# Performance work log

Measured on AMD Instinct MI355X. Metric: run time of the kernel, lower is better.

## Reference

```python
import jax, jax.numpy as jnp
import numpy as np

N_NODES = 50000
N_EDGES = 800000
N_GRAPHS = 512
IN_DIM = 128
HID = 256
K = 4
D4 = HID // K  # 64
OUT_DIM = 2
LN_EPS = 1e-5
BN_EPS = 1e-5


def elu(x):
    return jnp.where(x > 0, x, jnp.expm1(x))


def gin_conv(x, src, dst, n, W1, b1, W2, b2):
    # PyG GINConv, eps=0: mlp(x + sum_{j->i} x_j); mlp = Linear->ReLU->Linear
    agg = x + jax.ops.segment_sum(x[src], dst, num_segments=n)
    h = jnp.maximum(agg @ W1 + b1, 0.0)
    return h @ W2 + b2


def full_layernorm(x):
    # LayerNorm(normalized_shape=x.size(), elementwise_affine=False):
    # normalizes over the ENTIRE tensor (all nodes+features jointly)
    m = x.mean()
    v = x.var()  # biased, matches torch LayerNorm
    return (x - m) * jax.lax.rsqrt(v + LN_EPS)


def bn_eval(h):
    # BatchNorm1d in eval mode with fresh running stats (mean=0, var=1, affine=1/0)
    return h * jax.lax.rsqrt(jnp.float32(1.0) + BN_EPS)


def setup_inputs():
    key = jax.random.key(0)
    ks = jax.random.split(key, 24)
    rn = lambda k, shape, s=0.05: jax.random.normal(k, shape, dtype=jnp.float32) * s
    return {
        "x": jax.random.normal(ks[0], (N_NODES, IN_DIM), dtype=jnp.float32),
        "edge_index": jax.random.randint(ks[1], (2, N_EDGES), 0, N_NODES, dtype=jnp.int32),
        "batch": jnp.sort(jax.random.randint(ks[2], (N_NODES,), 0, N_GRAPHS, dtype=jnp.int32)),
        "lin1_W": rn(ks[3], (IN_DIM, HID)),
        "lin1_b": rn(ks[4], (HID,)),
        "gin0_W1": rn(ks[5], (HID, HID)),
        "gin0_b1": rn(ks[6], (HID,)),
        "gin0_W2": rn(ks[7], (HID, HID)),
        "gin0_b2": rn(ks[8], (HID,)),
        "gin1_W1": rn(ks[9], (K, D4, D4)),
        "gin1_b1": rn(ks[10], (K, D4)),
        "gin1_W2": rn(ks[11], (K, D4, D4)),
        "gin1_b2": rn(ks[12], (K, D4)),
        "vn_emb": jnp.zeros((HID,), dtype=jnp.float32),  # init constant 0
        "vn_W1": rn(ks[13], (HID, 2 * HID)),
        "vn_b1": rn(ks[14], (2 * HID,)),
        "vn_W2": rn(ks[15], (2 * HID, HID)),
        "vn_b2": rn(ks[16], (HID,)),
        "lin_out_W": rn(ks[17], (HID * 2 * 3, HID)),
        "lin_out_b": rn(ks[18], (HID,)),
        "cls_W": rn(ks[19], (HID, OUT_DIM)),
        "cls_b": rn(ks[20], (OUT_DIM,)),
        "dh_W": rn(ks[21], (3, D4)),
        "dh_b": rn(ks[22], (3,)),
    }


def reference(x, edge_index, batch, lin1_W, lin1_b,
              gin0_W1, gin0_b1, gin0_W2, gin0_b2,
              gin1_W1, gin1_b1, gin1_W2, gin1_b2,
              vn_emb, vn_W1, vn_b1, vn_W2, vn_b2,
              lin_out_W, lin_out_b, cls_W, cls_b, dh_W, dh_b):
    n = x.shape[0]
    # edge_attr is None -> add self loops
    src = jnp.concatenate([edge_index[0], jnp.arange(n, dtype=edge_index.dtype)])
    dst = jnp.concatenate([edge_index[1], jnp.arange(n, dtype=edge_index.dtype)])

    h = elu(x @ lin1_W + lin1_b)                       # [N, HID]
    vn = jnp.broadcast_to(vn_emb, (N_GRAPHS, HID))     # virtualnode embedding per graph

    gr = [h]
    # ---- layer 0: NaSingleOp (full-width GIN) ----
    orix = h
    h = h + vn[batch]
    h = gin_conv(h, src, dst, n, gin0_W1, gin0_b1, gin0_W2, gin0_b2)
    h = full_layernorm(elu(h))
    gr.append(h)
    # virtual node update (i < num_layers - 1)
    vt = jax.ops.segment_sum(orix, batch, num_segments=N_GRAPHS) + vn
    vn = jnp.maximum(bn_eval(vt @ vn_W1 + vn_b1), 0.0)
    vn = jnp.maximum(bn_eval(vn @ vn_W2 + vn_b2), 0.0)

    # ---- layer 1: NaDisenOp (4 quarter-width GINs on hsplit chunks) ----
    h = h + vn[batch]
    hk = h.reshape(n, K, D4)                           # hsplit(4)
    zk = jax.vmap(
        lambda xi, W1, b1, W2, b2: gin_conv(xi, src, dst, n, W1, b1, W2, b2),
        in_axes=(1, 0, 0, 0, 0), out_axes=1,
    )(hk, gin1_W1, gin1_b1, gin1_W2, gin1_b2)          # [N, K, D4]
    h = zk.reshape(n, HID)                             # hstack
    h = full_layernorm(elu(h))
    gr.append(h)

    gr = jnp.concatenate(gr, axis=1)                   # [N, 3*HID]

    # Pooling_trivial: passthrough. Readout_trivial: cat(max_pool, mean_pool)
    mx = jax.ops.segment_max(gr, batch, num_segments=N_GRAPHS)
    counts = jax.ops.segment_sum(jnp.ones((n,), dtype=gr.dtype), batch, num_segments=N_GRAPHS)
    mean = jax.ops.segment_sum(gr, batch, num_segments=N_GRAPHS) / jnp.maximum(counts, 1.0)[:, None]
    read = jnp.concatenate([mx, mean], axis=1)         # [G, 6*HID]

    x5 = elu(read @ lin_out_W + lin_out_b)             # [G, HID]

    # Disen3Head: first 3 of 4 hsplit chunks -> Linear(D4,1) -> 0.05+0.35*sigmoid
    xs = x5.reshape(N_GRAPHS, K, D4)
    z = jnp.einsum('gkd,kd->gk', xs[:, :3, :], dh_W) + dh_b
    ssl = 0.05 + 0.35 * jax.nn.sigmoid(z)              # [G, 3]

    logits = jax.nn.log_softmax(x5 @ cls_W + cls_b, axis=-1)  # mol=False
    return (logits, x5, ssl)
```

## Files before the change

### kernel.cpp

```cpp
#include <hip/hip_runtime.h>

static constexpr int NG = 512;
static constexpr float LN_EPS = 1e-5f;
static constexpr float BNS = 0.9999950000374997f;

__device__ __forceinline__ float eluf(float v) { return v > 0.f ? v : expm1f(v); }

typedef __attribute__((ext_vector_type(8))) short bf16x8;
typedef __attribute__((ext_vector_type(4))) float f32x4;

__device__ __forceinline__ ushort f2b(float f) {
    union { float f; unsigned u; } v; v.f = f;
    const unsigned u = v.u;
    return (ushort)((u + 0x7FFFu + ((u >> 16) & 1u)) >> 16);
}
__device__ __forceinline__ float b2f(ushort b) {
    union { unsigned u; float f; } v; v.u = ((unsigned)b) << 16;
    return v.f;
}

__device__ __forceinline__ void gl16(const ushort* g, ushort* l) {
    __builtin_amdgcn_global_load_lds(
        (const __attribute__((address_space(1))) void*)g,
        (__attribute__((address_space(3))) void*)l, 16, 0, 0);
}

template<int KSTEPS>
__global__ __launch_bounds__(512)
void tgemm_kernel(const ushort* __restrict__ Ab, int ldab,
                  const ushort* __restrict__ Wt,
                  const float* __restrict__ bias,
                  ushort* __restrict__ Cb,
                  int n)
{
    __shared__ __align__(16) ushort sbuf[32768];
    ushort* As = sbuf;
    ushort* Bs = sbuf + 8192;

    const int tid = threadIdx.x;
    const int lane = tid & 63;
    const int wv = tid >> 6;
    const int wr = wv >> 1, wc = wv & 1;
    const int r0 = blockIdx.x * 128;
    const int colL = lane & 15;
    const int lr = lane >> 4;

    f32x4 acc[2][8];
#pragma unroll
    for (int rt = 0; rt < 2; ++rt)
#pragma unroll
        for (int ct = 0; ct < 8; ++ct) acc[rt][ct] = (f32x4){0.f, 0.f, 0.f, 0.f};

    for (int ks = 0; ks < KSTEPS; ++ks) {
#pragma unroll
        for (int it = 0; it < 2; ++it) {
            const int i = it * 512 + tid;
            const int row = i >> 3, cb = i & 7;
            const int rg = min(r0 + row, n - 1);
            gl16(Ab + (size_t)rg * ldab + ks * 64 + ((cb ^ (row & 7)) * 8), As + i * 8);
        }
#pragma unroll
        for (int it = 0; it < 4; ++it) {
            const int i = it * 512 + tid;
            const int col = i >> 3, cb = i & 7;
            gl16(Wt + (size_t)col * (KSTEPS * 64) + ks * 64 + ((cb ^ (col & 7)) * 8), Bs + i * 8);
        }
        __syncthreads();

        bf16x8 af[2][2];
#pragma unroll
        for (int rt = 0; rt < 2; ++rt)
#pragma unroll
            for (int kk = 0; kk < 2; ++kk) {
                const int row = wr * 32 + rt * 16 + colL;
                const int blk = kk * 4 + lr;
                af[rt][kk] = *reinterpret_cast<const bf16x8*>(As + row * 64 + ((blk ^ (row & 7)) * 8));
            }
#pragma unroll
        for (int ct = 0; ct < 8; ++ct)
#pragma unroll
            for (int kk = 0; kk < 2; ++kk) {
                const int col = wc * 128 + ct * 16 + colL;
                const int blk = kk * 4 + lr;
                const bf16x8 bf = *reinterpret_cast<const bf16x8*>(Bs + col * 64 + ((blk ^ (col & 7)) * 8));
                acc[0][ct] = __builtin_amdgcn_mfma_f32_16x16x32_bf16(af[0][kk], bf, acc[0][ct], 0, 0, 0);
                acc[1][ct] = __builtin_amdgcn_mfma_f32_16x16x32_bf16(af[1][kk], bf, acc[1][ct], 0, 0, 0);
            }
        __syncthreads();
    }

    float bv[8];
#pragma unroll
    for (int ct = 0; ct < 8; ++ct) bv[ct] = bias[wc * 128 + ct * 16 + colL];

    ushort* eb = sbuf + wv * 4096;
#pragma unroll
    for (int rt = 0; rt < 2; ++rt)
#pragma unroll
        for (int ct = 0; ct < 8; ++ct)
#pragma unroll
            for (int r = 0; r < 4; ++r) {
                const float v = eluf(acc[rt][ct][r] + bv[ct]);
                eb[(rt * 16 + lr * 4 + r) * 128 + ct * 16 + colL] = f2b(v);
            }
#pragma unroll
    for (int j = 0; j < 8; ++j) {
        const int idx = j * 64 + lane;
        const int lrow = idx >> 4, c8 = idx & 15;
        const int grow = r0 + wr * 32 + lrow;
        if (grow < n)
            *reinterpret_cast<bf16x8*>(Cb + (size_t)grow * 256 + wc * 128 + c8 * 8) =
                *reinterpret_cast<const bf16x8*>(eb + lrow * 128 + c8 * 8);
    }
}

__global__ __launch_bounds__(512)
void mlp0_kernel(const ushort* __restrict__ Ab,
                 const ushort* __restrict__ W1t,
                 const ushort* __restrict__ W2t,
                 const float* __restrict__ b1, const float* __restrict__ b2,
                 ushort* __restrict__ Cb,
                 int n, double* __restrict__ stats)
{
    __shared__ __align__(16) ushort As[8192];
    __shared__ __align__(16) ushort Bs[16384];
    __shared__ __align__(16) ushort Z[32768];

    const int tid = threadIdx.x;
    const int lane = tid & 63;
    const int wv = tid >> 6;
    const int wr = wv >> 1, wc = wv & 1;
    const int r0 = blockIdx.x * 128;
    const int colL = lane & 15;
    const int lr = lane >> 4;

    f32x4 acc[2][8];
#pragma unroll
    for (int rt = 0; rt < 2; ++rt)
#pragma unroll
        for (int ct = 0; ct < 8; ++ct) acc[rt][ct] = (f32x4){0.f, 0.f, 0.f, 0.f};

    for (int ks = 0; ks < 4; ++ks) {
#pragma unroll
        for (int it = 0; it < 2; ++it) {
            const int i = it * 512 + tid;
            const int row = i >> 3, cb = i & 7;
            const int rg = min(r0 + row, n - 1);
            gl16(Ab + (size_t)rg * 256 + ks * 64 + ((cb ^ (row & 7)) * 8), As + i * 8);
        }
#pragma unroll
        for (int it = 0; it < 4; ++it) {
            const int i = it * 512 + tid;
            const int col = i >> 3, cb = i & 7;
            gl16(W1t + (size_t)col * 256 + ks * 64 + ((cb ^ (col & 7)) * 8), Bs + i * 8);
        }
        __syncthreads();
        bf16x8 af[2][2];
#pragma unroll
        for (int rt = 0; rt < 2; ++rt)
#pragma unroll
            for (int kk = 0; kk < 2; ++kk) {
                const int row = wr * 32 + rt * 16 + colL;
                const int blk = kk * 4 + lr;
                af[rt][kk] = *reinterpret_cast<const bf16x8*>(As + row * 64 + ((blk ^ (row & 7)) * 8));
            }
#pragma unroll
        for (int ct = 0; ct < 8; ++ct)
#pragma unroll
            for (int kk = 0; kk < 2; ++kk) {
                const int col = wc * 128 + ct * 16 + colL;
                const int blk = kk * 4 + lr;
                const bf16x8 bf = *reinterpret_cast<const bf16x8*>(Bs + col * 64 + ((blk ^ (col & 7)) * 8));
                acc[0][ct] = __builtin_amdgcn_mfma_f32_16x16x32_bf16(af[0][kk], bf, acc[0][ct], 0, 0, 0);
                acc[1][ct] = __builtin_amdgcn_mfma_f32_16x16x32_bf16(af[1][kk], bf, acc[1][ct], 0, 0, 0);
            }
        __syncthreads();
    }
#pragma unroll
    for (int ct = 0; ct < 8; ++ct) {
        const float bvv = b1[wc * 128 + ct * 16 + colL];
#pragma unroll
        for (int rt = 0; rt < 2; ++rt)
#pragma unroll
            for (int r = 0; r < 4; ++r) {
                const float v = fmaxf(acc[rt][ct][r] + bvv, 0.f);
                const int zrow = wr * 32 + rt * 16 + lr * 4 + r;
                const int zcol = wc * 128 + ct * 16 + colL;
                const int chunk = zcol >> 3;
                const int sw = (chunk & 24) | ((chunk & 7) ^ (zrow & 7));
                Z[zrow * 256 + sw * 8 + (zcol & 7)] = f2b(v);
            }
    }
    __syncthreads();

#pragma unroll
    for (int rt = 0; rt < 2; ++rt)
#pragma unroll
        for (int ct = 0; ct < 8; ++ct) acc[rt][ct] = (f32x4){0.f, 0.f, 0.f, 0.f};

    for (int ks = 0; ks < 4; ++ks) {
#pragma unroll
        for (int it = 0; it < 4; ++it) {
            const int i = it * 512 + tid;
            const int col = i >> 3, cb = i & 7;
            gl16(W2t + (size_t)col * 256 + ks * 64 + ((cb ^ (col & 7)) * 8), Bs + i * 8);
        }
        __syncthreads();
        bf16x8 zf[2][2];
#pragma unroll
        for (int rt = 0; rt < 2; ++rt)
#pragma unroll
            for (int kk = 0; kk < 2; ++kk) {
                const int zrow = wr * 32 + rt * 16 + colL;
                const int chunk = ks * 8 + kk * 4 + lr;
                const int sw = (chunk & 24) | ((chunk & 7) ^ (zrow & 7));
                zf[rt][kk] = *reinterpret_cast<const bf16x8*>(Z + zrow * 256 + sw * 8);
            }
#pragma unroll
        for (int ct = 0; ct < 8; ++ct)
#pragma unroll
            for (int kk = 0; kk < 2; ++kk) {
                const int col = wc * 128 + ct * 16 + colL;
                const int blk = kk * 4 + lr;
                const bf16x8 bf = *reinterpret_cast<const bf16x8*>(Bs + col * 64 + ((blk ^ (col & 7)) * 8));
                acc[0][ct] = __builtin_amdgcn_mfma_f32_16x16x32_bf16(zf[0][kk], bf, acc[0][ct], 0, 0, 0);
                acc[1][ct] = __builtin_amdgcn_mfma_f32_16x16x32_bf16(zf[1][kk], bf, acc[1][ct], 0, 0, 0);
            }
        __syncthreads();
    }

    float bv[8];
#pragma unroll
    for (int ct = 0; ct < 8; ++ct) bv[ct] = b2[wc * 128 + ct * 16 + colL];
    ushort* eb = Z + wv * 4096;
    float s = 0.f, ss = 0.f;
#pragma unroll
    for (int rt = 0; rt < 2; ++rt)
#pragma unroll
        for (int ct = 0; ct < 8; ++ct)
#pragma unroll
            for (int r = 0; r < 4; ++r) {
                const float v = eluf(acc[rt][ct][r] + bv[ct]);
                eb[(rt * 16 + lr * 4 + r) * 128 + ct * 16 + colL] = f2b(v);
                const int row = r0 + wr * 32 + rt * 16 + lr * 4 + r;
                if (row < n) { s += v; ss += v * v; }
            }
#pragma unroll
    for (int j = 0; j < 8; ++j) {
        const int idx = j * 64 + lane;
        const int lrow = idx >> 4, c8 = idx & 15;
        const int grow = r0 + wr * 32 + lrow;
        if (grow < n)
            *reinterpret_cast<bf16x8*>(Cb + (size_t)grow * 256 + wc * 128 + c8 * 8) =
                *reinterpret_cast<const bf16x8*>(eb + lrow * 128 + c8 * 8);
    }
    double ds = (double)s, dss = (double)ss;
    for (int o = 32; o; o >>= 1) { ds += __shfl_down(ds, o, 64); dss += __shfl_down(dss, o, 64); }
    if (lane == 0) {
        const int bkt = (blockIdx.x & 63) * 2;
        unsafeAtomicAdd(&stats[bkt], ds); unsafeAtomicAdd(&stats[bkt + 1], dss);
    }
}

__global__ __launch_bounds__(256)
void bd2_kernel(const ushort* __restrict__ Ab,
                const ushort* __restrict__ W1t,
                const ushort* __restrict__ W2t,
                const float* __restrict__ b1, const float* __restrict__ b2,
                ushort* __restrict__ Cb,
                int n, double* __restrict__ stats)
{
    __shared__ __align__(16) ushort As[8192];
    __shared__ __align__(16) ushort B1s[4096];
    __shared__ __align__(16) ushort B2s[4096];

    const int tid = threadIdx.x;
    const int lane = tid & 63;
    const int wv = tid >> 6;
    const int ch = blockIdx.y;
    const int r0 = blockIdx.x * 128;
    const int colL = lane & 15;
    const int lr = lane >> 4;

#pragma unroll
    for (int it = 0; it < 4; ++it) {
        const int i = it * 256 + tid;
        const int row = i >> 3, cb = i & 7;
        const int rg = min(r0 + row, n - 1);
        gl16(Ab + (size_t)rg * 256 + ch * 64 + ((cb ^ (row & 7)) * 8), As + i * 8);
    }
#pragma unroll
    for (int it = 0; it < 2; ++it) {
        const int i = it * 256 + tid;
        const int col = i >> 3, cb = i & 7;
        gl16(W1t + ch * 4096 + col * 64 + ((cb ^ (col & 7)) * 8), B1s + i * 8);
    }
#pragma unroll
    for (int it = 0; it < 2; ++it) {
        const int i = it * 256 + tid;
        const int col = i >> 3, cb = i & 7;
        gl16(W2t + ch * 4096 + col * 64 + ((cb ^ (col & 7)) * 8), B2s + i * 8);
    }
    __syncthreads();

    bf16x8 af[2][2];
#pragma unroll
    for (int rt = 0; rt < 2; ++rt)
#pragma unroll
        for (int kk = 0; kk < 2; ++kk) {
            const int row = wv * 32 + rt * 16 + colL;
            const int blk = kk * 4 + lr;
            af[rt][kk] = *reinterpret_cast<const bf16x8*>(As + row * 64 + ((blk ^ (row & 7)) * 8));
        }
    f32x4 acc[2][4];
#pragma unroll
    for (int rt = 0; rt < 2; ++rt)
#pragma unroll
        for (int ct = 0; ct < 4; ++ct) acc[rt][ct] = (f32x4){0.f, 0.f, 0.f, 0.f};
#pragma unroll
    for (int ct = 0; ct < 4; ++ct)
#pragma unroll
        for (int kk = 0; kk < 2; ++kk) {
            const int col = ct * 16 + colL;
            const int blk = kk * 4 + lr;
            const bf16x8 bf = *reinterpret_cast<const bf16x8*>(B1s + col * 64 + ((blk ^ (col & 7)) * 8));
            acc[0][ct] = __builtin_amdgcn_mfma_f32_16x16x32_bf16(af[0][kk], bf, acc[0][ct], 0, 0, 0);
            acc[1][ct] = __builtin_amdgcn_mfma_f32_16x16x32_bf16(af[1][kk], bf, acc[1][ct], 0, 0, 0);
        }

    ushort* Zw = As + wv * 2048;
#pragma unroll
    for (int rt = 0; rt < 2; ++rt)
#pragma unroll
        for (int ct = 0; ct < 4; ++ct) {
            const float bvv = b1[ch * 64 + ct * 16 + colL];
#pragma unroll
            for (int r = 0; r < 4; ++r) {
                const float v = fmaxf(acc[rt][ct][r] + bvv, 0.f);
                const int zrow = rt * 16 + lr * 4 + r;
                const int zcol = ct * 16 + colL;
                Zw[zrow * 64 + (((zcol >> 3) ^ (zrow & 7)) * 8) + (zcol & 7)] = f2b(v);
            }
        }

    bf16x8 zf[2][2];
#pragma unroll
    for (int rt = 0; rt < 2; ++rt)
#pragma unroll
        for (int kk = 0; kk < 2; ++kk) {
            const int zrow = rt * 16 + colL;
            const int blk = kk * 4 + lr;
            zf[rt][kk] = *reinterpret_cast<const bf16x8*>(Zw + zrow * 64 + ((blk ^ (zrow & 7)) * 8));
        }
#pragma unroll
    for (int rt = 0; rt < 2; ++rt)
#pragma unroll
        for (int ct = 0; ct < 4; ++ct) acc[rt][ct] = (f32x4){0.f, 0.f, 0.f, 0.f};
#pragma unroll
    for (int ct = 0; ct < 4; ++ct)
#pragma unroll
        for (int kk = 0; kk < 2; ++kk) {
            const int col = ct * 16 + colL;
            const int blk = kk * 4 + lr;
            const bf16x8 bf = *reinterpret_cast<const bf16x8*>(B2s + col * 64 + ((blk ^ (col & 7)) * 8));
            acc[0][ct] = __builtin_amdgcn_mfma_f32_16x16x32_bf16(zf[0][kk], bf, acc[0][ct], 0, 0, 0);
            acc[1][ct] = __builtin_amdgcn_mfma_f32_16x16x32_bf16(zf[1][kk], bf, acc[1][ct], 0, 0, 0);
        }

    float s = 0.f, ss = 0.f;
#pragma unroll
    for (int rt = 0; rt < 2; ++rt)
#pragma unroll
        for (int ct = 0; ct < 4; ++ct) {
            const float bvv = b2[ch * 64 + ct * 16 + colL];
#pragma unroll
            for (int r = 0; r < 4; ++r) {
                const float v = eluf(acc[rt][ct][r] + bvv);
                Zw[(rt * 16 + lr * 4 + r) * 64 + ct * 16 + colL] = f2b(v);
                const int row = r0 + wv * 32 + rt * 16 + lr * 4 + r;
                if (row < n) { s += v; ss += v * v; }
            }
        }
#pragma unroll
    for (int j = 0; j < 4; ++j) {
        const int idx = j * 64 + lane;
        const int lrow = idx >> 3, c8 = idx & 7;
        const int grow = r0 + wv * 32 + lrow;
        if (grow < n)
            *reinterpret_cast<bf16x8*>(Cb + (size_t)grow * 256 + ch * 64 + c8 * 8) =
                *reinterpret_cast<const bf16x8*>(Zw + lrow * 64 + c8 * 8);
    }

    double ds = (double)s, dss = (double)ss;
    for (int o = 32; o; o >>= 1) { ds += __shfl_down(ds, o, 64); dss += __shfl_down(dss, o, 64); }
    if (lane == 0) {
        const int bkt = ((blockIdx.x + blockIdx.y * 16) & 63) * 2;
        unsafeAtomicAdd(&stats[bkt], ds); unsafeAtomicAdd(&stats[bkt + 1], dss);
    }
}

__global__ __launch_bounds__(64)
void finalize_kernel(const double* __restrict__ sacc, float* __restrict__ sfin, double M)
{
    const int t = threadIdx.x;
    double s = sacc[t * 2], ss = sacc[t * 2 + 1];
    for (int o = 32; o; o >>= 1) { s += __shfl_down(s, o, 64); ss += __shfl_down(ss, o, 64); }
    if (t == 0) {
        const double mean = s / M;
        double var = ss / M - mean * mean;
        if (var < 0.0) var = 0.0;
        sfin[0] = (float)mean;
        sfin[1] = (float)(1.0 / sqrt(var + (double)LN_EPS));
    }
}

__global__ void prep_kernel(const float* __restrict__ x,
                            const float* __restrict__ lin1W,
                            const float* __restrict__ g0W1, const float* __restrict__ g0W2,
                            const float* __restrict__ g1W1, const float* __restrict__ g1W2,
                            ushort* __restrict__ xb,
                            ushort* __restrict__ Wt1,
                            ushort* __restrict__ Wt0a, ushort* __restrict__ Wt0b,
                            ushort* __restrict__ Wtbd1, ushort* __restrict__ Wtbd2,
                            int n32)
{
    const int i = blockIdx.x * 256 + threadIdx.x;
    if (i < n32) {
        const float4 v = reinterpret_cast<const float4*>(x)[i];
        reinterpret_cast<ushort4*>(xb)[i] = make_ushort4(f2b(v.x), f2b(v.y), f2b(v.z), f2b(v.w));
        return;
    }
    int j = i - n32;
    if (j < 32768) {
        const int c = j >> 7, k = j & 127;
        Wt1[j] = f2b(lin1W[(size_t)k * 256 + c]);
    } else if (j < 98304) {
        j -= 32768;
        const int c = j >> 8, k = j & 255;
        Wt0a[j] = f2b(g0W1[(size_t)k * 256 + c]);
    } else if (j < 163840) {
        j -= 98304;
        const int c = j >> 8, k = j & 255;
        Wt0b[j] = f2b(g0W2[(size_t)k * 256 + c]);
    } else if (j < 180224) {
        j -= 163840;
        const int ch = j >> 12, r = j & 4095, cw = r >> 6, k = r & 63;
        Wtbd1[j] = f2b(g1W1[ch * 4096 + k * 64 + cw]);
    } else if (j < 196608) {
        j -= 180224;
        const int ch = j >> 12, r = j & 4095, cw = r >> 6, k = r & 63;
        Wtbd2[j] = f2b(g1W2[ch * 4096 + k * 64 + cw]);
    }
}

__global__ void count_kernel(const int* __restrict__ dst, int* __restrict__ cnt, int nE)
{
    const int e = blockIdx.x * 256 + threadIdx.x;
    if (e < nE) atomicAdd(&cnt[dst[e]], 1);
}

__global__ __launch_bounds__(256)
void scan1_kernel(const int* __restrict__ cnt, int* __restrict__ bsum, int n)
{
    __shared__ int ws[4];
    const int i = blockIdx.x * 256 + threadIdx.x;
    int v = (i < n) ? cnt[i] : 0;
    for (int o = 32; o; o >>= 1) v += __shfl_down(v, o, 64);
    if ((threadIdx.x & 63) == 0) ws[threadIdx.x >> 6] = v;
    __syncthreads();
    if (threadIdx.x == 0) bsum[blockIdx.x] = ws[0] + ws[1] + ws[2] + ws[3];
}

__global__ __launch_bounds__(256)
void scan2_kernel(int* __restrict__ bsum, int* __restrict__ rowptr, int nb, int n)
{
    __shared__ int sh[256];
    const int t = threadIdx.x;
    const int v = (t < nb) ? bsum[t] : 0;
    sh[t] = v;
    __syncthreads();
    for (int o = 1; o < 256; o <<= 1) {
        const int u = (t >= o) ? sh[t - o] : 0;
        __syncthreads();
        sh[t] += u;
        __syncthreads();
    }
    if (t < nb) bsum[t] = sh[t] - v;
    if (t == 255) rowptr[n] = sh[255];
}

__global__ __launch_bounds__(256)
void scan3_kernel(const int* __restrict__ cnt, const int* __restrict__ bsum,
                  int* __restrict__ rowptr, int* __restrict__ cursor, int n)
{
    __shared__ int sh[256];
    const int t = threadIdx.x;
    const int i = blockIdx.x * 256 + t;
    const int v = (i < n) ? cnt[i] : 0;
    sh[t] = v;
    __syncthreads();
    for (int o = 1; o < 256; o <<= 1) {
        const int u = (t >= o) ? sh[t - o] : 0;
        __syncthreads();
        sh[t] += u;
        __syncthreads();
    }
    if (i < n) {
        const int ex = bsum[blockIdx.x] + sh[t] - v;
        rowptr[i] = ex;
        cursor[i] = ex;
    }
}

__global__ void fill_kernel(const int* __restrict__ src, const int* __restrict__ dst,
                            int* __restrict__ cursor, int* __restrict__ es, int nE)
{
    const int e = blockIdx.x * 256 + threadIdx.x;
    if (e >= nE) return;
    const int p = atomicAdd(&cursor[dst[e]], 1);
    es[p] = src[e];
}

__global__ __launch_bounds__(256)
void gather0b_kernel(const ushort* __restrict__ hb, const int* __restrict__ rowptr,
                     const int* __restrict__ es, const float* __restrict__ vn_emb,
                     ushort* __restrict__ ob, int n)
{
    const int node = blockIdx.x * 4 + (threadIdx.x >> 6);
    if (node >= n) return;
    const int lane = threadIdx.x & 63;
    const ushort4* H4 = reinterpret_cast<const ushort4*>(hb);
    const ushort4 o = H4[(size_t)node * 64 + lane];
    const int b = rowptr[node], e = rowptr[node + 1];
    const float4 vn = reinterpret_cast<const float4*>(vn_emb)[lane];
    const float cv = (float)(2 + (e - b));
    float a0 = fmaf(cv, vn.x, 2.f * b2f(o.x));
    float a1 = fmaf(cv, vn.y, 2.f * b2f(o.y));
    float a2 = fmaf(cv, vn.z, 2.f * b2f(o.z));
    float a3 = fmaf(cv, vn.w, 2.f * b2f(o.w));
    int i = b;
    for (; i + 2 <= e; i += 2) {
        const ushort4 v0 = H4[(size_t)es[i] * 64 + lane];
        const ushort4 v1 = H4[(size_t)es[i + 1] * 64 + lane];
        a0 += b2f(v0.x) + b2f(v1.x);
        a1 += b2f(v0.y) + b2f(v1.y);
        a2 += b2f(v0.z) + b2f(v1.z);
        a3 += b2f(v0.w) + b2f(v1.w);
    }
    for (; i < e; ++i) {
        const ushort4 v = H4[(size_t)es[i] * 64 + lane];
        a0 += b2f(v.x); a1 += b2f(v.y); a2 += b2f(v.z); a3 += b2f(v.w);
    }
    reinterpret_cast<ushort4*>(ob)[(size_t)node * 64 + lane] =
        make_ushort4(f2b(a0), f2b(a1), f2b(a2), f2b(a3));
}

__global__ __launch_bounds__(256)
void gatherb_kernel(const ushort* __restrict__ tb, const int* __restrict__ rowptr,
                    const int* __restrict__ es, ushort* __restrict__ ob, int n)
{
    const int node = blockIdx.x * 4 + (threadIdx.x >> 6);
    if (node >= n) return;
    const int lane = threadIdx.x & 63;
    const ushort4* H4 = reinterpret_cast<const ushort4*>(tb);
    const ushort4 o = H4[(size_t)node * 64 + lane];
    float a0 = 2.f * b2f(o.x), a1 = 2.f * b2f(o.y), a2 = 2.f * b2f(o.z), a3 = 2.f * b2f(o.w);
    const int b = rowptr[node], e = rowptr[node + 1];
    int i = b;
    for (; i + 2 <= e; i += 2) {
        const ushort4 v0 = H4[(size_t)es[i] * 64 + lane];
        const ushort4 v1 = H4[(size_t)es[i + 1] * 64 + lane];
        a0 += b2f(v0.x) + b2f(v1.x);
        a1 += b2f(v0.y) + b2f(v1.y);
        a2 += b2f(v0.z) + b2f(v1.z);
        a3 += b2f(v0.w) + b2f(v1.w);
    }
    for (; i < e; ++i) {
        const ushort4 v = H4[(size_t)es[i] * 64 + lane];
        a0 += b2f(v.x); a1 += b2f(v.y); a2 += b2f(v.z); a3 += b2f(v.w);
    }
    reinterpret_cast<ushort4*>(ob)[(size_t)node * 64 + lane] =
        make_ushort4(f2b(a0), f2b(a1), f2b(a2), f2b(a3));
}

__global__ void offsets_kernel(const int* __restrict__ batch, int n, int* __restrict__ off)
{
    const int g = blockIdx.x * blockDim.x + threadIdx.x;
    if (g > NG) return;
    int lo = 0, hi = n;
    while (lo < hi) { const int mid = (lo + hi) >> 1; if (batch[mid] < g) lo = mid + 1; else hi = mid; }
    off[g] = lo;
}

__global__ void norm0f_kernel(const ushort* __restrict__ zb, const float* __restrict__ sfin,
                              const float* __restrict__ vn2, const int* __restrict__ batch,
                              ushort* __restrict__ grs, ushort* __restrict__ tb, int n)
{
    const size_t i4 = (size_t)blockIdx.x * blockDim.x + threadIdx.x;
    if (i4 >= (size_t)n * 64) return;
    const float m = sfin[0], rs = sfin[1];
    const int row = (int)(i4 >> 6), c4 = (int)(i4 & 63);
    const ushort4 u = reinterpret_cast<const ushort4*>(zb)[i4];
    const float z0 = (b2f(u.x) - m) * rs, z1 = (b2f(u.y) - m) * rs,
                z2 = (b2f(u.z) - m) * rs, z3 = (b2f(u.w) - m) * rs;
    reinterpret_cast<ushort4*>(grs)[(size_t)row * 128 + c4] =
        make_ushort4(f2b(z0), f2b(z1), f2b(z2), f2b(z3));
    const int g = batch[row];
    const float4 e = reinterpret_cast<const float4*>(vn2 + (size_t)g * 256)[c4];
    reinterpret_cast<ushort4*>(tb)[i4] =
        make_ushort4(f2b(z0 + e.x), f2b(z1 + e.y), f2b(z2 + e.z), f2b(z3 + e.w));
}

__global__ void norm1b_kernel(const ushort* __restrict__ zb, const float* __restrict__ sfin,
                              ushort* __restrict__ grs, int n)
{
    const size_t i4 = (size_t)blockIdx.x * blockDim.x + threadIdx.x;
    if (i4 >= (size_t)n * 64) return;
    const float m = sfin[0], rs = sfin[1];
    const int row = (int)(i4 >> 6), c4 = (int)(i4 & 63);
    const ushort4 u = reinterpret_cast<const ushort4*>(zb)[i4];
    reinterpret_cast<ushort4*>(grs)[(size_t)row * 128 + 64 + c4] =
        make_ushort4(f2b((b2f(u.x) - m) * rs), f2b((b2f(u.y) - m) * rs),
                     f2b((b2f(u.z) - m) * rs), f2b((b2f(u.w) - m) * rs));
}

__global__ __launch_bounds__(256)
void vnall_kernel(const ushort* __restrict__ hb, const int* __restrict__ off,
                  const float* __restrict__ vn_emb,
                  const float* __restrict__ W1, const float* __restrict__ bb1,
                  const float* __restrict__ W2, const float* __restrict__ bb2,
                  float* __restrict__ vn2)
{
    __shared__ float r1[256];
    __shared__ float r2[512];
    const int g = blockIdx.x, t = threadIdx.x;
    const int i0 = off[g], i1 = off[g + 1];
    float s = 0.f;
    for (int i = i0; i < i1; ++i) s += b2f(hb[(size_t)i * 256 + t]);
    r1[t] = s + vn_emb[t];
    __syncthreads();
    float a0 = 0.f, a1 = 0.f;
    for (int k = 0; k < 256; ++k) {
        const float rv = r1[k];
        a0 = fmaf(rv, W1[(size_t)k * 512 + t], a0);
        a1 = fmaf(rv, W1[(size_t)k * 512 + 256 + t], a1);
    }
    r2[t]       = fmaxf((a0 + bb1[t]) * BNS, 0.f);
    r2[t + 256] = fmaxf((a1 + bb1[256 + t]) * BNS, 0.f);
    __syncthreads();
    float a = 0.f;
    for (int k = 0; k < 512; ++k) a = fmaf(r2[k], W2[(size_t)k * 256 + t], a);
    vn2[(size_t)g * 256 + t] = fmaxf((a + bb2[t]) * BNS, 0.f);
}

__global__ __launch_bounds__(256)
void pool_kernel(const ushort* __restrict__ hb, const ushort* __restrict__ g2,
                 const int* __restrict__ off, float* __restrict__ readb)
{
    const int g = blockIdx.x, t = threadIdx.x;
    const int i0 = off[g], i1 = off[g + 1];
    float m0 = -__builtin_inff(), m1 = m0, m2 = m0;
    float s0 = 0.f, s1 = 0.f, s2 = 0.f;
    for (int i = i0; i < i1; ++i) {
        const float v0 = b2f(hb[(size_t)i * 256 + t]);
        const ushort2 z = *reinterpret_cast<const ushort2*>(g2 + (size_t)i * 512 + 2 * t);
        const float v1 = b2f(z.x), v2 = b2f(z.y);
        m0 = fmaxf(m0, v0); m1 = fmaxf(m1, v1); m2 = fmaxf(m2, v2);
        s0 += v0; s1 += v1; s2 += v2;
    }
    const float inv = 1.f / fmaxf((float)(i1 - i0), 1.f);
    float* rb = readb + (size_t)g * 1536;
    rb[t] = m0;
    rb[256 + 2 * t] = m1; rb[256 + 2 * t + 1] = m2;
    rb[768 + t] = s0 * inv;
    rb[1024 + 2 * t] = s1 * inv; rb[1024 + 2 * t + 1] = s2 * inv;
}

__global__ __launch_bounds__(256)
void outg2_kernel(const float* __restrict__ readb, const float* __restrict__ W,
                  const float* __restrict__ b,
                  const float* __restrict__ clsW, const float* __restrict__ clsb,
                  const float* __restrict__ dW, const float* __restrict__ db,
                  float* __restrict__ x5, float* __restrict__ logits, float* __restrict__ ssl)
{
    __shared__ float rows[2][1536];
    __shared__ float x5s[2][256];
    const int g0 = blockIdx.x * 2, t = threadIdx.x;
    for (int i = t; i < 2 * 1536; i += 256) rows[i / 1536][i % 1536] = readb[(size_t)g0 * 1536 + i];
    __syncthreads();
    float a0 = 0.f, a1 = 0.f;
    for (int k = 0; k < 1536; ++k) {
        const float wv = W[(size_t)k * 256 + t];
        a0 = fmaf(rows[0][k], wv, a0);
        a1 = fmaf(rows[1][k], wv, a1);
    }
    const float bb = b[t];
    const float v0 = eluf(a0 + bb), v1 = eluf(a1 + bb);
    x5[(size_t)g0 * 256 + t] = v0;
    x5[(size_t)(g0 + 1) * 256 + t] = v1;
    x5s[0][t] = v0;
    x5s[1][t] = v1;
    __syncthreads();

    const int grp = t >> 5, l32 = t & 31;
    if (grp < 2) {
        float p0 = 0.f, p1 = 0.f;
        for (int c = l32; c < 256; c += 32) {
            const float v = x5s[grp][c];
            p0 = fmaf(v, clsW[c * 2], p0);
            p1 = fmaf(v, clsW[c * 2 + 1], p1);
        }
        float q0 = 0.f, q1 = 0.f, q2 = 0.f;
        for (int c = l32; c < 64; c += 32) {
            q0 = fmaf(x5s[grp][c],       dW[c],       q0);
            q1 = fmaf(x5s[grp][64 + c],  dW[64 + c],  q1);
            q2 = fmaf(x5s[grp][128 + c], dW[128 + c], q2);
        }
        for (int o = 16; o; o >>= 1) {
            p0 += __shfl_down(p0, o, 32); p1 += __shfl_down(p1, o, 32);
            q0 += __shfl_down(q0, o, 32); q1 += __shfl_down(q1, o, 32); q2 += __shfl_down(q2, o, 32);
        }
        if (l32 == 0) {
            const float z0 = p0 + clsb[0], z1 = p1 + clsb[1];
            const float m = fmaxf(z0, z1);
            const float lse = m + logf(expf(z0 - m) + expf(z1 - m));
            logits[(size_t)(g0 + grp) * 2 + 0] = z0 - lse;
            logits[(size_t)(g0 + grp) * 2 + 1] = z1 - lse;
            ssl[(size_t)(g0 + grp) * 3 + 0] = 0.05f + 0.35f / (1.f + expf(-(q0 + db[0])));
            ssl[(size_t)(g0 + grp) * 3 + 1] = 0.05f + 0.35f / (1.f + expf(-(q1 + db[1])));
            ssl[(size_t)(g0 + grp) * 3 + 2] = 0.05f + 0.35f / (1.f + expf(-(q2 + db[2])));
        }
    }
}

extern "C" void kernel_launch(void* const* d_in, const int* in_sizes, int n_in,
                              void* d_out, int out_size, void* d_ws, size_t ws_size,
                              hipStream_t stream)
{
    const float* x      = (const float*)d_in[0];
    const int*   eidx   = (const int*)d_in[1];
    const int*   batch  = (const int*)d_in[2];
    const float* lin1_W = (const float*)d_in[3];
    const float* lin1_b = (const float*)d_in[4];
    const float* g0W1   = (const float*)d_in[5];
    const float* g0b1   = (const float*)d_in[6];
    const float* g0W2   = (const float*)d_in[7];
    const float* g0b2   = (const float*)d_in[8];
    const float* g1W1   = (const float*)d_in[9];
    const float* g1b1   = (const float*)d_in[10];
    const float* g1W2   = (const float*)d_in[11];
    const float* g1b2   = (const float*)d_in[12];
    const float* vn_emb = (const float*)d_in[13];
    const float* vnW1   = (const float*)d_in[14];
    const float* vnb1   = (const float*)d_in[15];
    const float* vnW2   = (const float*)d_in[16];
    const float* vnb2   = (const float*)d_in[17];
    const float* loW    = (const float*)d_in[18];
    const float* lob    = (const float*)d_in[19];
    const float* clsW   = (const float*)d_in[20];
    const float* clsb   = (const float*)d_in[21];
    const float* dhW    = (const float*)d_in[22];
    const float* dhb    = (const float*)d_in[23];

    const int N = in_sizes[2];
    const int E = in_sizes[1] / 2;
    const int* esrc = eidx;
    const int* edst = eidx + E;

    float* out = (float*)d_out;
    float* out_logits = out;
    float* out_x5     = out + (size_t)NG * 2;
    float* out_ssl    = out + (size_t)NG * 2 + (size_t)NG * 256;

    char* p = (char*)d_ws;
    auto carve = [&](size_t bytes) { char* r = p; p += (bytes + 255) & ~(size_t)255; return (void*)r; };
    double* sacc   = (double*)carve(256 * sizeof(double));
    int*    cnt    = (int*)   carve((size_t)N * sizeof(int));
    float*  sfin   = (float*) carve(4 * sizeof(float));
    int*    goff   = (int*)   carve((NG + 1) * sizeof(int));
    int*    rowptr = (int*)   carve((size_t)(N + 1) * sizeof(int));
    int*    cursor = (int*)   carve((size_t)N * sizeof(int));
    int*    bsum   = (int*)   carve(256 * sizeof(int));
    int*    es     = (int*)   carve((size_t)E * sizeof(int));
    ushort* gr2    = (ushort*)carve((size_t)N * 512 * sizeof(ushort));
    ushort* xb     = (ushort*)carve((size_t)N * 128 * sizeof(ushort));
    ushort* B1     = (ushort*)carve((size_t)N * 256 * sizeof(ushort));
    ushort* B2     = (ushort*)carve((size_t)N * 256 * sizeof(ushort));
    ushort* B3     = (ushort*)carve((size_t)N * 256 * sizeof(ushort));
    ushort* Wt1    = (ushort*)carve(256 * 128 * sizeof(ushort));
    ushort* Wt0a   = (ushort*)carve(256 * 256 * sizeof(ushort));
    ushort* Wt0b   = (ushort*)carve(256 * 256 * sizeof(ushort));
    ushort* Wtbd1  = (ushort*)carve(16384 * sizeof(ushort));
    ushort* Wtbd2  = (ushort*)carve(16384 * sizeof(ushort));
    float*  vn2    = (float*) carve((size_t)NG * 256 * sizeof(float));
    float*  readb  = (float*) carve((size_t)NG * 1536 * sizeof(float));

    hipMemsetAsync(sacc, 0, 2048 + (size_t)N * sizeof(int), stream);

    const int mt = (N + 127) / 128;
    const int vecGrid = (N * 64 + 255) / 256;
    const int eGrid = (E + 255) / 256;
    const int gatherGrid = (N + 3) / 4;
    const int nb = (N + 255) / 256;
    const int prepTotal = N * 32 + 196608;

    count_kernel<<<eGrid, 256, 0, stream>>>(edst, cnt, E);
    scan1_kernel<<<nb, 256, 0, stream>>>(cnt, bsum, N);
    scan2_kernel<<<1, 256, 0, stream>>>(bsum, rowptr, nb, N);
    scan3_kernel<<<nb, 256, 0, stream>>>(cnt, bsum, rowptr, cursor, N);
    fill_kernel<<<eGrid, 256, 0, stream>>>(esrc, edst, cursor, es, E);

    prep_kernel<<<(prepTotal + 255) / 256, 256, 0, stream>>>(
        x, lin1_W, g0W1, g0W2, g1W1, g1W2, xb, Wt1, Wt0a, Wt0b, Wtbd1, Wtbd2, N * 32);

    tgemm_kernel<2><<<mt, 512, 0, stream>>>(xb, 128, Wt1, lin1_b, B1, N);
    offsets_kernel<<<3, 256, 0, stream>>>(batch, N, goff);

    vnall_kernel<<<NG, 256, 0, stream>>>(B1, goff, vn_emb, vnW1, vnb1, vnW2, vnb2, vn2);

    gather0b_kernel<<<gatherGrid, 256, 0, stream>>>(B1, rowptr, es, vn_emb, B2, N);
    mlp0_kernel<<<mt, 512, 0, stream>>>(B2, Wt0a, Wt0b, g0b1, g0b2, B3, N, sacc);
    finalize_kernel<<<1, 64, 0, stream>>>(sacc, sfin, (double)N * 256.0);
    norm0f_kernel<<<vecGrid, 256, 0, stream>>>(B3, sfin, vn2, batch, gr2, B2, N);

    gatherb_kernel<<<gatherGrid, 256, 0, stream>>>(B2, rowptr, es, B3, N);
    bd2_kernel<<<dim3(mt, 4), 256, 0, stream>>>(B3, Wtbd1, Wtbd2, g1b1, g1b2, B2, N, sacc + 128);
    finalize_kernel<<<1, 64, 0, stream>>>(sacc + 128, sfin + 2, (double)N * 256.0);
    norm1b_kernel<<<vecGrid, 256, 0, stream>>>(B2, sfin + 2, gr2, N);

    pool_kernel<<<NG, 256, 0, stream>>>(B1, gr2, goff, readb);
    outg2_kernel<<<NG / 2, 256, 0, stream>>>(readb, loW, lob, clsW, clsb, dhW, dhb,
                                             out_x5, out_logits, out_ssl);
}
```

Baseline: 512.4 us.

## Run output linear layer on bf16 MFMA GEMM and split classifier head

Replaces the scalar fp32 outg2 kernel (512x1536 by 1536x256 matvec-style loops over 256 blocks) with the existing MFMA tile GEMM, templated to write fp32 output directly. The pooled readout is now stored as bf16 and the lin_out weight is transposed and converted to bf16 in the prep kernel. A small per-graph head kernel then computes the log-softmax logits and the ssl sigmoids from x5. This trades fp32 precision on the readout and weights for tensor-core throughput, but the GEMM runs on only 4 blocks, which may leave much of the GPU idle.

```diff
diff --git a/kernel.cpp b/kernel.cpp
--- a/kernel.cpp
+++ b/kernel.cpp
@@ -25,12 +25,12 @@
         (__attribute__((address_space(3))) void*)l, 16, 0, 0);
 }
 
-template<int KSTEPS>
+template<int KSTEPS, bool WB16, bool WF32>
 __global__ __launch_bounds__(512)
 void tgemm_kernel(const ushort* __restrict__ Ab, int ldab,
                   const ushort* __restrict__ Wt,
                   const float* __restrict__ bias,
-                  ushort* __restrict__ Cb,
+                  ushort* __restrict__ Cb, float* __restrict__ Cf,
                   int n)
 {
     __shared__ __align__(16) ushort sbuf[32768];
@@ -101,16 +101,24 @@
 #pragma unroll
             for (int r = 0; r < 4; ++r) {
                 const float v = eluf(acc[rt][ct][r] + bv[ct]);
-                eb[(rt * 16 + lr * 4 + r) * 128 + ct * 16 + colL] = f2b(v);
-            }
-#pragma unroll
-    for (int j = 0; j < 8; ++j) {
-        const int idx = j * 64 + lane;
-        const int lrow = idx >> 4, c8 = idx & 15;
-        const int grow = r0 + wr * 32 + lrow;
-        if (grow < n)
-            *reinterpret_cast<bf16x8*>(Cb + (size_t)grow * 256 + wc * 128 + c8 * 8) =
-                *reinterpret_cast<const bf16x8*>(eb + lrow * 128 + c8 * 8);
+                if constexpr (WB16)
+                    eb[(rt * 16 + lr * 4 + r) * 128 + ct * 16 + colL] = f2b(v);
+                if constexpr (WF32) {
+                    const int row = r0 + wr * 32 + rt * 16 + lr * 4 + r;
+                    const int col = wc * 128 + ct * 16 + colL;
+                    if (row < n) Cf[(size_t)row * 256 + col] = v;
+                }
+            }
+    if constexpr (WB16) {
+#pragma unroll
+        for (int j = 0; j < 8; ++j) {
+            const int idx = j * 64 + lane;
+            const int lrow = idx >> 4, c8 = idx & 15;
+            const int grow = r0 + wr * 32 + lrow;
+            if (grow < n)
+                *reinterpret_cast<bf16x8*>(Cb + (size_t)grow * 256 + wc * 128 + c8 * 8) =
+                    *reinterpret_cast<const bf16x8*>(eb + lrow * 128 + c8 * 8);
+        }
     }
 }
 
@@ -418,10 +426,12 @@
                             const float* __restrict__ lin1W,
                             const float* __restrict__ g0W1, const float* __restrict__ g0W2,
                             const float* __restrict__ g1W1, const float* __restrict__ g1W2,
+                            const float* __restrict__ loW,
                             ushort* __restrict__ xb,
                             ushort* __restrict__ Wt1,
                             ushort* __restrict__ Wt0a, ushort* __restrict__ Wt0b,
                             ushort* __restrict__ Wtbd1, ushort* __restrict__ Wtbd2,
+                            ushort* __restrict__ loWt,
                             int n32)
 {
     const int i = blockIdx.x * 256 + threadIdx.x;
@@ -450,6 +460,10 @@
         j -= 180224;
         const int ch = j >> 12, r = j & 4095, cw = r >> 6, k = r & 63;
         Wtbd2[j] = f2b(g1W2[ch * 4096 + k * 64 + cw]);
+    } else if (j < 196608 + 393216) {
+        j -= 196608;
+        const int c = j / 1536, k = j - c * 1536;
+        loWt[j] = f2b(loW[(size_t)k * 256 + c]);
     }
 }
 
@@ -655,7 +669,7 @@
 
 __global__ __launch_bounds__(256)
 void pool_kernel(const ushort* __restrict__ hb, const ushort* __restrict__ g2,
-                 const int* __restrict__ off, float* __restrict__ readb)
+                 const int* __restrict__ off, ushort* __restrict__ readbb)
 {
     const int g = blockIdx.x, t = threadIdx.x;
     const int i0 = off[g], i1 = off[g + 1];
@@ -669,67 +683,42 @@
         s0 += v0; s1 += v1; s2 += v2;
     }
     const float inv = 1.f / fmaxf((float)(i1 - i0), 1.f);
-    float* rb = readb + (size_t)g * 1536;
-    rb[t] = m0;
-    rb[256 + 2 * t] = m1; rb[256 + 2 * t + 1] = m2;
-    rb[768 + t] = s0 * inv;
-    rb[1024 + 2 * t] = s1 * inv; rb[1024 + 2 * t + 1] = s2 * inv;
-}
-
-__global__ __launch_bounds__(256)
-void outg2_kernel(const float* __restrict__ readb, const float* __restrict__ W,
-                  const float* __restrict__ b,
-                  const float* __restrict__ clsW, const float* __restrict__ clsb,
-                  const float* __restrict__ dW, const float* __restrict__ db,
-                  float* __restrict__ x5, float* __restrict__ logits, float* __restrict__ ssl)
-{
-    __shared__ float rows[2][1536];
-    __shared__ float x5s[2][256];
-    const int g0 = blockIdx.x * 2, t = threadIdx.x;
-    for (int i = t; i < 2 * 1536; i += 256) rows[i / 1536][i % 1536] = readb[(size_t)g0 * 1536 + i];
-    __syncthreads();
-    float a0 = 0.f, a1 = 0.f;
-    for (int k = 0; k < 1536; ++k) {
-        const float wv = W[(size_t)k * 256 + t];
-        a0 = fmaf(rows[0][k], wv, a0);
-        a1 = fmaf(rows[1][k], wv, a1);
-    }
-    const float bb = b[t];
-    const float v0 = eluf(a0 + bb), v1 = eluf(a1 + bb);
-    x5[(size_t)g0 * 256 + t] = v0;
-    x5[(size_t)(g0 + 1) * 256 + t] = v1;
-    x5s[0][t] = v0;
-    x5s[1][t] = v1;
-    __syncthreads();
-
-    const int grp = t >> 5, l32 = t & 31;
-    if (grp < 2) {
-        float p0 = 0.f, p1 = 0.f;
-        for (int c = l32; c < 256; c += 32) {
-            const float v = x5s[grp][c];
-            p0 = fmaf(v, clsW[c * 2], p0);
-            p1 = fmaf(v, clsW[c * 2 + 1], p1);
-        }
-        float q0 = 0.f, q1 = 0.f, q2 = 0.f;
-        for (int c = l32; c < 64; c += 32) {
-            q0 = fmaf(x5s[grp][c],       dW[c],       q0);
-            q1 = fmaf(x5s[grp][64 + c],  dW[64 + c],  q1);
-            q2 = fmaf(x5s[grp][128 + c], dW[128 + c], q2);
-        }
-        for (int o = 16; o; o >>= 1) {
-            p0 += __shfl_down(p0, o, 32); p1 += __shfl_down(p1, o, 32);
-            q0 += __shfl_down(q0, o, 32); q1 += __shfl_down(q1, o, 32); q2 += __shfl_down(q2, o, 32);
-        }
-        if (l32 == 0) {
-            const float z0 = p0 + clsb[0], z1 = p1 + clsb[1];
-            const float m = fmaxf(z0, z1);
-            const float lse = m + logf(expf(z0 - m) + expf(z1 - m));
-            logits[(size_t)(g0 + grp) * 2 + 0] = z0 - lse;
-            logits[(size_t)(g0 + grp) * 2 + 1] = z1 - lse;
-            ssl[(size_t)(g0 + grp) * 3 + 0] = 0.05f + 0.35f / (1.f + expf(-(q0 + db[0])));
-            ssl[(size_t)(g0 + grp) * 3 + 1] = 0.05f + 0.35f / (1.f + expf(-(q1 + db[1])));
-            ssl[(size_t)(g0 + grp) * 3 + 2] = 0.05f + 0.35f / (1.f + expf(-(q2 + db[2])));
-        }
+    ushort* rb = readbb + (size_t)g * 1536;
+    rb[t] = f2b(m0);
+    rb[256 + 2 * t] = f2b(m1); rb[256 + 2 * t + 1] = f2b(m2);
+    rb[768 + t] = f2b(s0 * inv);
+    rb[1024 + 2 * t] = f2b(s1 * inv); rb[1024 + 2 * t + 1] = f2b(s2 * inv);
+}
+
+__global__ __launch_bounds__(64)
+void head_kernel(const float* __restrict__ x5, const float* __restrict__ clsW,
+                 const float* __restrict__ clsb, const float* __restrict__ dW,
+                 const float* __restrict__ db, float* __restrict__ logits,
+                 float* __restrict__ ssl)
+{
+    const int g = blockIdx.x, l = threadIdx.x;
+    const float* xg = x5 + (size_t)g * 256;
+    const float4 v   = reinterpret_cast<const float4*>(xg)[l];
+    const float4 w01 = reinterpret_cast<const float4*>(clsW)[l * 2];
+    const float4 w23 = reinterpret_cast<const float4*>(clsW)[l * 2 + 1];
+    float p0 = v.x * w01.x + v.y * w01.z + v.z * w23.x + v.w * w23.z;
+    float p1 = v.x * w01.y + v.y * w01.w + v.z * w23.y + v.w * w23.w;
+    float q0 = xg[l] * dW[l];
+    float q1 = xg[64 + l] * dW[64 + l];
+    float q2 = xg[128 + l] * dW[128 + l];
+    for (int o = 32; o; o >>= 1) {
+        p0 += __shfl_down(p0, o, 64); p1 += __shfl_down(p1, o, 64);
+        q0 += __shfl_down(q0, o, 64); q1 += __shfl_down(q1, o, 64); q2 += __shfl_down(q2, o, 64);
+    }
+    if (l == 0) {
+        const float z0 = p0 + clsb[0], z1 = p1 + clsb[1];
+        const float m = fmaxf(z0, z1);
+        const float lse = m + logf(expf(z0 - m) + expf(z1 - m));
+        logits[(size_t)g * 2 + 0] = z0 - lse;
+        logits[(size_t)g * 2 + 1] = z1 - lse;
+        ssl[(size_t)g * 3 + 0] = 0.05f + 0.35f / (1.f + expf(-(q0 + db[0])));
+        ssl[(size_t)g * 3 + 1] = 0.05f + 0.35f / (1.f + expf(-(q1 + db[1])));
+        ssl[(size_t)g * 3 + 2] = 0.05f + 0.35f / (1.f + expf(-(q2 + db[2])));
     }
 }
 
@@ -792,8 +781,9 @@
     ushort* Wt0b   = (ushort*)carve(256 * 256 * sizeof(ushort));
     ushort* Wtbd1  = (ushort*)carve(16384 * sizeof(ushort));
     ushort* Wtbd2  = (ushort*)carve(16384 * sizeof(ushort));
+    ushort* loWt   = (ushort*)carve(256 * 1536 * sizeof(ushort));
     float*  vn2    = (float*) carve((size_t)NG * 256 * sizeof(float));
-    float*  readb  = (float*) carve((size_t)NG * 1536 * sizeof(float));
+    ushort* readbb = (ushort*)carve((size_t)NG * 1536 * sizeof(ushort));
 
     hipMemsetAsync(sacc, 0, 2048 + (size_t)N * sizeof(int), stream);
 
@@ -802,7 +792,7 @@
     const int eGrid = (E + 255) / 256;
     const int gatherGrid = (N + 3) / 4;
     const int nb = (N + 255) / 256;
-    const int prepTotal = N * 32 + 196608;
+    const int prepTotal = N * 32 + 196608 + 393216;
 
     count_kernel<<<eGrid, 256, 0, stream>>>(edst, cnt, E);
     scan1_kernel<<<nb, 256, 0, stream>>>(cnt, bsum, N);
@@ -811,9 +801,10 @@
     fill_kernel<<<eGrid, 256, 0, stream>>>(esrc, edst, cursor, es, E);
 
     prep_kernel<<<(prepTotal + 255) / 256, 256, 0, stream>>>(
-        x, lin1_W, g0W1, g0W2, g1W1, g1W2, xb, Wt1, Wt0a, Wt0b, Wtbd1, Wtbd2, N * 32);
-
-    tgemm_kernel<2><<<mt, 512, 0, stream>>>(xb, 128, Wt1, lin1_b, B1, N);
+        x, lin1_W, g0W1, g0W2, g1W1, g1W2, loW,
+        xb, Wt1, Wt0a, Wt0b, Wtbd1, Wtbd2, loWt, N * 32);
+
+    tgemm_kernel<2, true, false><<<mt, 512, 0, stream>>>(xb, 128, Wt1, lin1_b, B1, nullptr, N);
     offsets_kernel<<<3, 256, 0, stream>>>(batch, N, goff);
 
     vnall_kernel<<<NG, 256, 0, stream>>>(B1, goff, vn_emb, vnW1, vnb1, vnW2, vnb2, vn2);
@@ -828,7 +819,8 @@
     finalize_kernel<<<1, 64, 0, stream>>>(sacc + 128, sfin + 2, (double)N * 256.0);
     norm1b_kernel<<<vecGrid, 256, 0, stream>>>(B2, sfin + 2, gr2, N);
 
-    pool_kernel<<<NG, 256, 0, stream>>>(B1, gr2, goff, readb);
-    outg2_kernel<<<NG / 2, 256, 0, stream>>>(readb, loW, lob, clsW, clsb, dhW, dhb,
-                                             out_x5, out_logits, out_ssl);
-}
+    pool_kernel<<<NG, 256, 0, stream>>>(B1, gr2, goff, readbb);
+    tgemm_kernel<24, false, true><<<(NG + 127) / 128, 512, 0, stream>>>(
+        readbb, 1536, loWt, lob, nullptr, out_x5, NG);
+    head_kernel<<<NG, 64, 0, stream>>>(out_x5, clsW, clsb, dhW, dhb, out_logits, out_ssl);
+}
```

After: 504.3 us. Within noise of the previous version (-1.6%).
